# Performance work log

Measured on AMD Instinct MI355X. Metric: run time of the kernel, lower is better.

## Reference

```python
import jax, jax.numpy as jnp
import numpy as np

B, S, HID = 2, 2048, 2048
H, HKV, D = 16, 8, 128
CHUNK = 512
THETA = 1000000.0
NEG = -1e9


def setup_inputs() -> dict:
    key = jax.random.key(0)
    ks = jax.random.split(key, 10)
    hidden_states = jax.random.normal(ks[0], (B, S, HID), dtype=jnp.float32)
    # additive causal mask (0 on/below diagonal, -1e9 above)
    tri = jnp.tril(jnp.ones((S, S), dtype=bool))
    attention_mask = jnp.where(tri, 0.0, NEG).astype(jnp.float32)
    attention_mask = jnp.broadcast_to(attention_mask[None, None], (B, 1, S, S))
    w = 0.02
    Wq = jax.random.normal(ks[1], (HID, H * D), dtype=jnp.float32) * w
    bq = jax.random.normal(ks[2], (H * D,), dtype=jnp.float32) * w
    Wk = jax.random.normal(ks[3], (HID, HKV * D), dtype=jnp.float32) * w
    bk = jax.random.normal(ks[4], (HKV * D,), dtype=jnp.float32) * w
    Wv = jax.random.normal(ks[5], (HID, HKV * D), dtype=jnp.float32) * w
    bv = jax.random.normal(ks[6], (HKV * D,), dtype=jnp.float32) * w
    Wo = jax.random.normal(ks[7], (H * D, HID), dtype=jnp.float32) * w
    bo = jax.random.normal(ks[8], (HID,), dtype=jnp.float32) * w
    return {"hidden_states": hidden_states, "attention_mask": attention_mask,
            "Wq": Wq, "bq": bq, "Wk": Wk, "bk": bk, "Wv": Wv, "bv": bv,
            "Wo": Wo, "bo": bo}


def _rope_tables(seq_len, dim):
    inv_freq = 1.0 / (THETA ** (jnp.arange(0, dim, 2, dtype=jnp.float32) / dim))
    pos = jnp.arange(seq_len, dtype=jnp.float32)
    freqs = pos[:, None] * inv_freq[None, :]          # [S, D/2]
    emb = jnp.concatenate([freqs, freqs], axis=-1)    # [S, D]
    return jnp.cos(emb)[None, None], jnp.sin(emb)[None, None]  # [1,1,S,D]


def _rotate_half(x):
    x1, x2 = jnp.split(x, 2, axis=-1)
    return jnp.concatenate([-x2, x1], axis=-1)


def _attn_forward(hidden_states, attention_mask, Wq, bq, Wk, bk, Wv, bv, Wo, bo):
    bsz, s, _ = hidden_states.shape
    q = (hidden_states @ Wq + bq).reshape(bsz, s, H, D).transpose(0, 2, 1, 3)
    k = (hidden_states @ Wk + bk).reshape(bsz, s, HKV, D).transpose(0, 2, 1, 3)
    v = (hidden_states @ Wv + bv).reshape(bsz, s, HKV, D).transpose(0, 2, 1, 3)
    cos, sin = _rope_tables(s, D)
    q = q * cos + _rotate_half(q) * sin
    k = k * cos + _rotate_half(k) * sin
    n_rep = H // HKV
    k = jnp.repeat(k, n_rep, axis=1)  # repeat_kv
    v = jnp.repeat(v, n_rep, axis=1)
    scale = 1.0 / jnp.sqrt(jnp.float32(D))
    nq, nk = s // CHUNK, s // CHUNK
    Qc = q.reshape(bsz, H, nq, CHUNK, D)
    Kc = jnp.moveaxis(k.reshape(bsz, H, nk, CHUNK, D), 2, 0)   # [nk,B,H,Ck,D]
    Vc = jnp.moveaxis(v.reshape(bsz, H, nk, CHUNK, D), 2, 0)
    Mc = jnp.moveaxis(attention_mask.reshape(bsz, 1, nq, CHUNK, nk, CHUNK), 4, 0)  # [nk,B,1,nq,Cq,Ck]

    def step(carry, xs):
        o, m, d = carry
        k_seg, v_seg, m_seg = xs
        # scores: [B,H,nq,Cq,Ck]
        sc = jnp.einsum('bhqcd,bhkd->bhqck', Qc, k_seg) * scale + m_seg
        new_m = jnp.maximum(m, sc.max(axis=-1, keepdims=True))
        e = jnp.exp(sc - new_m)
        sums = e.sum(axis=-1, keepdims=True)
        prev = jnp.exp(m - new_m)          # NOTE: uses running max, as in source
        d_new = prev + sums
        o = (o * prev + jnp.einsum('bhqck,bhkd->bhqcd', e, v_seg)) / d_new
        return (o, new_m, d_new), None

    o0 = jnp.zeros((bsz, H, nq, CHUNK, D), dtype=jnp.float32)
    m0 = jnp.full((bsz, H, nq, CHUNK, 1), -jnp.inf, dtype=jnp.float32)
    d0 = jnp.ones((bsz, H, nq, CHUNK, 1), dtype=jnp.float32)
    (o, m, d), _ = jax.lax.scan(step, (o0, m0, d0), (Kc, Vc, Mc))
    # final rescale: attn_output * exp(max - logsumexp) == o / d_last (source math)
    o = o / d
    attn = o.reshape(bsz, H, s, D).transpose(0, 2, 1, 3).reshape(bsz, s, H * D)
    return attn @ Wo + bo


def reference(hidden_states, attention_mask, Wq, bq, Wk, bk, Wv, bv, Wo, bo):
    return _attn_forward(hidden_states, attention_mask, Wq, bq, Wk, bk, Wv, bv, Wo, bo)
```

## Files before the change

### kernel.cpp

```cpp
#include <hip/hip_runtime.h>
#include <hip/hip_bf16.h>


typedef __attribute__((ext_vector_type(8))) short s8v;
typedef __attribute__((ext_vector_type(4))) float f4v;
typedef __attribute__((ext_vector_type(4))) unsigned int u32x4;

#define MFMA16(a, b, c) __builtin_amdgcn_mfma_f32_16x16x32_bf16((a), (b), (c), 0, 0, 0)

typedef unsigned short u16;
typedef const __attribute__((address_space(1))) unsigned int* gas_p;
typedef __attribute__((address_space(3))) unsigned int* las_p;

__device__ __forceinline__ void gl_lds16(const void* g, void* l) {
    __builtin_amdgcn_global_load_lds((gas_p)g, (las_p)l, 16, 0, 0);
}

__device__ __forceinline__ u16 f2b(float f) {
    __hip_bfloat16 h = __float2bfloat16(f);
    return *reinterpret_cast<u16*>(&h);
}
__device__ __forceinline__ float b2f(u16 u) {
    __hip_bfloat16 h;
    *reinterpret_cast<u16*>(&h) = u;
    return __bfloat162float(h);
}

__device__ __forceinline__ void qswap(unsigned int& a, unsigned int& b) {
#if __has_builtin(__builtin_amdgcn_permlane32_swap) && __has_builtin(__builtin_amdgcn_permlane16_swap)
    typedef __attribute__((ext_vector_type(2))) unsigned int u32x2;
    u32x2 r1 = __builtin_amdgcn_permlane32_swap(a, b, false, false);
    u32x2 r2 = __builtin_amdgcn_permlane16_swap(r1[0], r1[1], false, false);
    a = r2[0]; b = r2[1];
#else
    asm volatile("v_permlane32_swap_b32 %0, %1\n\t"
                 "s_nop 0\n\t"
                 "v_permlane16_swap_b32 %0, %1\n\t"
                 "s_nop 0"
                 : "+v"(a), "+v"(b));
#endif
}

__device__ const unsigned char qt_tab[40] = {
    4, 5, 6, 7,
    8, 8, 9, 9, 10, 10, 11, 11,
    12, 12, 12, 13, 13, 13, 14, 14, 14, 15, 15, 15,
    3, 7, 11, 15, 2, 6, 10, 14, 1, 5, 9, 13, 0, 4, 8, 12};
__device__ const unsigned char c_tab[40] = {
    0, 0, 0, 0,
    0, 1, 0, 1, 0, 1, 0, 1,
    0, 1, 2, 0, 1, 2, 0, 1, 2, 0, 1, 2,
    0, 1, 2, 3, 0, 1, 2, 3, 0, 1, 2, 3, 0, 1, 2, 3};

__device__ __forceinline__ int uoff40(int qt, int c) {
    int qc = qt >> 2;
    if (c < qc) {
        if (qt < 8) return qt - 4;
        if (qt < 12) return 4 + ((qt - 8) << 1) + c;
        return 12 + (qt - 12) * 3 + c;
    }
    return 24 + ((3 - (qt & 3)) << 2) + qc;
}

__global__ __launch_bounds__(256) void k_cast_hs(const float* __restrict__ src,
                                                 u16* __restrict__ dst) {
    int i = blockIdx.x * 256 + threadIdx.x;
    float4 v = reinterpret_cast<const float4*>(src)[i];
    alignas(8) u16 t[4] = {f2b(v.x), f2b(v.y), f2b(v.z), f2b(v.w)};
    reinterpret_cast<uint2*>(dst)[i] = *reinterpret_cast<uint2*>(t);
}

__global__ __launch_bounds__(256) void k_transpose_w(
    const float* __restrict__ Wq, const float* __restrict__ Wk,
    const float* __restrict__ Wv, const float* __restrict__ Wo,
    u16* __restrict__ wt_all, u16* __restrict__ wo_t) {
    int id = blockIdx.x;
    const float* W; u16* dst; int N, nbase;
    if (id < 4096)      { W = Wq; dst = wt_all; N = 2048; nbase = 0; }
    else if (id < 6144) { W = Wk; dst = wt_all; N = 1024; nbase = 2048; id -= 4096; }
    else if (id < 8192) { W = Wv; dst = wt_all; N = 1024; nbase = 3072; id -= 6144; }
    else                { W = Wo; dst = wo_t;  N = 2048; nbase = 0;    id -= 8192; }
    int tiles_n = N >> 5;
    int k0 = (id / tiles_n) << 5, n0 = (id % tiles_n) << 5;
    __shared__ float t[32][33];
    int tid = threadIdx.x;
    {
        int row = tid >> 3, c4 = (tid & 7) << 2;
        float4 v = *reinterpret_cast<const float4*>(&W[(size_t)(k0 + row) * N + n0 + c4]);
        t[row][c4 + 0] = v.x; t[row][c4 + 1] = v.y;
        t[row][c4 + 2] = v.z; t[row][c4 + 3] = v.w;
    }
    __syncthreads();
    {
        int n = tid >> 3, kq = (tid & 7) << 2;
        alignas(8) u16 p[4];
#pragma unroll
        for (int j = 0; j < 4; j++) p[j] = f2b(t[kq + j][n]);
        *reinterpret_cast<uint2*>(&dst[(size_t)(nbase + n0 + n) * 2048 + k0 + kq]) =
            *reinterpret_cast<uint2*>(p);
    }
}

__global__ __launch_bounds__(256) void k_bias(const float* __restrict__ bq,
                                              const float* __restrict__ bk,
                                              const float* __restrict__ bv,
                                              float* __restrict__ dst) {
    int i = blockIdx.x * 256 + threadIdx.x;
    float v = (i < 2048) ? bq[i] : (i < 3072) ? bk[i - 2048] : bv[i - 3072];
    dst[i] = v;
}

__global__ __launch_bounds__(256) void k_gemm(
    const u16* __restrict__ A, const u16* __restrict__ Bt,
    const float* __restrict__ bias, void* __restrict__ out,
    int M, int N, int K, int out_f32) {
    __shared__ alignas(16) u16 As[128][64];
    __shared__ alignas(16) u16 Bs[128][64];
    int tid = threadIdx.x;
    int wave = tid >> 6, lane = tid & 63, quad = lane >> 4, l16 = lane & 15;
    int m0 = blockIdx.y << 7, n0 = blockIdx.x << 7;
    int wm = (wave >> 1) << 6, wn = (wave & 1) << 6;
    f4v zero = {0.f, 0.f, 0.f, 0.f};
    f4v acc[4][4];
#pragma unroll
    for (int a = 0; a < 4; a++)
#pragma unroll
        for (int b = 0; b < 4; b++) acc[a][b] = zero;
    int r0 = tid >> 3;
    int gsw = (tid & 7) ^ (r0 & 7);
    const u16* gA = A + (size_t)(m0 + r0) * K + (gsw << 3);
    const u16* gB = Bt + (size_t)(n0 + r0) * K + (gsw << 3);
    for (int k0 = 0; k0 < K; k0 += 64) {
        __syncthreads();
#pragma unroll
        for (int i = 0; i < 4; i++) {
            gl_lds16(gA + (size_t)(i << 5) * K + k0, (char*)As + (i << 12) + tid * 16);
            gl_lds16(gB + (size_t)(i << 5) * K + k0, (char*)Bs + (i << 12) + tid * 16);
        }
        __syncthreads();
#pragma unroll
        for (int ks = 0; ks < 2; ks++) {
            int rg = (((ks << 2) | quad) ^ (l16 & 7)) << 3;
            s8v af[4], bf_[4];
#pragma unroll
            for (int mi = 0; mi < 4; mi++)
                af[mi] = *reinterpret_cast<const s8v*>(&As[wm + mi * 16 + l16][rg]);
#pragma unroll
            for (int ni = 0; ni < 4; ni++)
                bf_[ni] = *reinterpret_cast<const s8v*>(&Bs[wn + ni * 16 + l16][rg]);
#pragma unroll
            for (int mi = 0; mi < 4; mi++)
#pragma unroll
                for (int ni = 0; ni < 4; ni++)
                    acc[mi][ni] = MFMA16(af[mi], bf_[ni], acc[mi][ni]);
        }
    }
#pragma unroll
    for (int mi = 0; mi < 4; mi++) {
#pragma unroll
        for (int ni = 0; ni < 4; ni++) {
            int n = n0 + wn + ni * 16 + l16;
            float bsv = bias[n];
#pragma unroll
            for (int r = 0; r < 4; r++) {
                int m = m0 + wm + mi * 16 + (quad << 2) + r;
                float v = acc[mi][ni][r] + bsv;
                if (out_f32)
                    reinterpret_cast<float*>(out)[(size_t)m * N + n] = v;
                else
                    reinterpret_cast<u16*>(out)[(size_t)m * N + n] = f2b(v);
            }
        }
    }
}

__global__ __launch_bounds__(256) void k_rope(const u16* __restrict__ qkv,
                                              u16* __restrict__ qr,
                                              u16* __restrict__ kr) {
    const float qscale = 0.08838834764831845f * 1.44269504088896340f;
    int row = blockIdx.x;
    int b = row >> 11, s = row & 2047;
    const u16* src = qkv + (size_t)row * 4096;
    __shared__ float lcs[64], lsn[64];
    int tid = threadIdx.x;
    if (tid < 64) {
        float fr = (float)s * exp2f((float)tid * -0.31143075889569023f);
        lcs[tid] = cosf(fr);
        lsn[tid] = sinf(fr);
    }
    __syncthreads();
    for (int u = tid; u < 1536; u += 256) {
        int hh, i;
        const u16* sp;
        u16* dp;
        float sc;
        if (u < 1024) {
            hh = u >> 6; i = u & 63;
            sp = src + hh * 128;
            dp = qr + ((size_t)(b * 16 + hh) * 2048 + s) * 128;
            sc = qscale;
        } else {
            int u2 = u - 1024;
            hh = u2 >> 6; i = u2 & 63;
            sp = src + 2048 + hh * 128;
            dp = kr + ((size_t)(b * 8 + hh) * 2048 + s) * 128;
            sc = 1.f;
        }
        float x1 = b2f(sp[i]);
        float x2 = b2f(sp[i + 64]);
        float cs = lcs[i], sn = lsn[i];
        dp[i]      = f2b((x1 * cs - x2 * sn) * sc);
        dp[i + 64] = f2b((x2 * cs + x1 * sn) * sc);
    }
}

__global__ __launch_bounds__(256) void k_vtrans(const u16* __restrict__ qkv,
                                                u16* __restrict__ vt) {
    int bkv = blockIdx.z, b = bkv >> 3, kv = bkv & 7;
    int s0 = blockIdx.x << 6, d0 = blockIdx.y << 5;
    __shared__ alignas(16) u16 t[32][72];
    int tid = threadIdx.x, c = tid & 31, rr = tid >> 5;
#pragma unroll
    for (int i = 0; i < 8; i++) {
        int s = s0 + rr + i * 8;
        t[c][rr + i * 8] = qkv[(size_t)(b * 2048 + s) * 4096 + 3072 + kv * 128 + d0 + c];
    }
    __syncthreads();
    int dd = tid >> 3, sc8 = (tid & 7) << 3;
    *reinterpret_cast<uint4*>(&vt[((size_t)(b * 8 + kv) * 128 + d0 + dd) * 2048 + s0 + sc8]) =
        *reinterpret_cast<const uint4*>(&t[dd][sc8]);
}

__global__ __launch_bounds__(256) void k_attn_part(const u16* __restrict__ qr,
                                                   const u16* __restrict__ kr,
                                                   const u16* __restrict__ vt,
                                                   u16* __restrict__ PVp,
                                                   float* __restrict__ scp) {
    const float NINF = -__builtin_inff();
    __shared__ alignas(16) u16 Ks[2][64 * 128];
    __shared__ alignas(16) u16 Vs[2][128 * 64];

    int tid = threadIdx.x;
    int wv = tid >> 6, lane = tid & 63, quad = lane >> 4, l16 = lane & 15;
    int x = blockIdx.x, h = blockIdx.y, b = blockIdx.z, kvh = h >> 1;
    int qt = qt_tab[x], c = c_tab[x], qc = qt >> 2;
    bool diag = (c == qc);
    int m3 = qt & 3;
    int nt = diag ? ((m3 + 1) << 1) : 8;
    int kbase = c << 9;
    const u16* Qp = qr + ((size_t)(b * 16 + h) * 2048 + qt * 128 + wv * 32) * 128;
    const u16* Kp = kr + ((size_t)(b * 8 + kvh) * 2048) * 128;
    const u16* Vp = vt + ((size_t)(b * 8 + kvh) * 128) * 2048;

    s8v qf0[4], qf1[4];
#pragma unroll
    for (int sl = 0; sl < 4; sl++) {
        qf0[sl] = *reinterpret_cast<const s8v*>(&Qp[l16 * 128 + sl * 32 + (quad << 3)]);
        qf1[sl] = *reinterpret_cast<const s8v*>(&Qp[(16 + l16) * 128 + sl * 32 + (quad << 3)]);
    }
    s8v ones;
#pragma unroll
    for (int i = 0; i < 8; i++) ones[i] = (short)0x3F80;

    int krow = tid >> 4, kg = (tid & 15) ^ krow;
    int vd = tid >> 3, vg = (tid & 7) ^ (vd & 7);
    auto stage = [&](int t) {
        int kbt = kbase + (t << 6);
        const u16* kgp = Kp + (size_t)(kbt + krow) * 128 + (kg << 3);
        const u16* vgp = Vp + (size_t)vd * 2048 + kbt + (vg << 3);
        char* kd = (char*)&Ks[t & 1][0];
        char* vdst = (char*)&Vs[t & 1][0];
#pragma unroll
        for (int i = 0; i < 4; i++) {
            gl_lds16(kgp + (size_t)(i << 4) * 128, kd + (i << 12) + tid * 16);
            gl_lds16(vgp + (size_t)(i << 5) * 2048, vdst + (i << 12) + tid * 16);
        }
    };

    auto pack = [&](const f4v& s, bool tri, bool act, float& tmx,
                    unsigned int& wlo, unsigned int& whi) {
        if (!act) { wlo = 0u; whi = 0u; return; }
        float e[4];
#pragma unroll
        for (int r = 0; r < 4; r++) {
            float v = s[r];
            if (tri && ((quad << 2) + r > l16)) v = NINF;
            tmx = fmaxf(tmx, v);
            e[r] = __builtin_amdgcn_exp2f(v);
        }
        wlo = (unsigned int)f2b(e[0]) | ((unsigned int)f2b(e[1]) << 16);
        whi = (unsigned int)f2b(e[2]) | ((unsigned int)f2b(e[3]) << 16);
    };

    f4v zero = {0.f, 0.f, 0.f, 0.f};
    f4v u0[8], u1[8], sums0 = zero, sums1 = zero;
#pragma unroll
    for (int ni = 0; ni < 8; ni++) { u0[ni] = zero; u1[ni] = zero; }
    float tmx0 = NINF, tmx1 = NINF;
    int qg0 = wv << 1, qg1 = (wv << 1) + 1;

    stage(0);
    for (int t = 0; t < nt; t++) {
        __syncthreads();
        if (t + 1 < nt) stage(t + 1);
        const char* Kbuf = (const char*)&Ks[t & 1][0];
        const char* Vbuf = (const char*)&Vs[t & 1][0];
        int kgb = diag ? ((t << 2) - (m3 << 3)) : -1000;

#pragma unroll
        for (int s2 = 0; s2 < 2; s2++) {
            int kgA = kgb + (s2 << 1);
            if (kgA > qg1) continue;
            int kgB = kgA + 1;
            bool a0 = (kgA <= qg0), b0 = (kgB <= qg0), b1 = (kgB <= qg1);
            f4v sA0 = zero, sA1 = zero, sB0 = zero, sB1 = zero;
#pragma unroll
            for (int sl = 0; sl < 4; sl++) {
                s8v kf = *reinterpret_cast<const s8v*>(
                    Kbuf + (((s2 << 1) << 4) + l16) * 256 +
                    ((((sl << 2) + quad) ^ l16) << 4));
                if (a0) sA0 = MFMA16(kf, qf0[sl], sA0);
                sA1 = MFMA16(kf, qf1[sl], sA1);
            }
            if (b1) {
#pragma unroll
                for (int sl = 0; sl < 4; sl++) {
                    s8v kf = *reinterpret_cast<const s8v*>(
                        Kbuf + ((((s2 << 1) | 1) << 4) + l16) * 256 +
                        ((((sl << 2) + quad) ^ l16) << 4));
                    if (b0) sB0 = MFMA16(kf, qf0[sl], sB0);
                    sB1 = MFMA16(kf, qf1[sl], sB1);
                }
            }
            unsigned int A0w, A1w, B0w, B1w;
            pack(sA1, kgA == qg1, true, tmx1, A0w, A1w);
            pack(sB1, kgB == qg1, b1, tmx1, B0w, B1w);
            qswap(A0w, B0w); qswap(A1w, B1w);
            u32x4 pw1 = {A0w, A1w, B0w, B1w};
            s8v pa1 = __builtin_bit_cast(s8v, pw1);
            sums1 = MFMA16(pa1, ones, sums1);
            s8v pa0 = pa1;
            if (a0) {
                unsigned int C0w, C1w, D0w, D1w;
                pack(sA0, kgA == qg0, true, tmx0, C0w, C1w);
                pack(sB0, kgB == qg0, b0, tmx0, D0w, D1w);
                qswap(C0w, D0w); qswap(C1w, D1w);
                u32x4 pw0 = {C0w, C1w, D0w, D1w};
                pa0 = __builtin_bit_cast(s8v, pw0);
                sums0 = MFMA16(pa0, ones, sums0);
            }
#pragma unroll
            for (int ni = 0; ni < 8; ni++) {
                s8v vf = *reinterpret_cast<const s8v*>(
                    Vbuf + ((ni << 4) + l16) * 128 +
                    ((((s2 << 2) + quad) ^ (l16 & 7)) << 4));
                if (a0) u0[ni] = MFMA16(pa0, vf, u0[ni]);
                u1[ni] = MFMA16(pa1, vf, u1[ni]);
            }
        }
    }
    tmx0 = fmaxf(tmx0, __shfl_xor(tmx0, 16));
    tmx0 = fmaxf(tmx0, __shfl_xor(tmx0, 32));
    tmx1 = fmaxf(tmx1, __shfl_xor(tmx1, 16));
    tmx1 = fmaxf(tmx1, __shfl_xor(tmx1, 32));
    float m0[4], m1[4], resc0[4], resc1[4];
#pragma unroll
    for (int r = 0; r < 4; r++) {
        m0[r] = __shfl(tmx0, (quad << 2) + r);
        m1[r] = __shfl(tmx1, (quad << 2) + r);
        resc0[r] = __builtin_amdgcn_exp2f(-m0[r]);
        resc1[r] = __builtin_amdgcn_exp2f(-m1[r]);
    }
    int slot = (b * 16 + h) * 40 + x;
    u16* pvdst = PVp + (size_t)slot * 16384;
    int row0 = wv * 32 + (quad << 2);
#pragma unroll
    for (int ni = 0; ni < 8; ni++)
#pragma unroll
        for (int r = 0; r < 4; r++) {
            pvdst[(row0 + r) * 128 + ni * 16 + l16] = f2b(u0[ni][r] * resc0[r]);
            pvdst[(row0 + 16 + r) * 128 + ni * 16 + l16] = f2b(u1[ni][r] * resc1[r]);
        }
    if (l16 == 0) {
        float* scd = scp + (size_t)slot * 256 + row0;
#pragma unroll
        for (int r = 0; r < 4; r++) {
            scd[r] = m0[r] * 0.6931471805599453f;
            scd[16 + r] = m1[r] * 0.6931471805599453f;
            scd[128 + r] = sums0[r] * resc0[r];
            scd[144 + r] = sums1[r] * resc1[r];
        }
    }
}

__global__ __launch_bounds__(256) void k_attn_comb(const u16* __restrict__ PVp,
                                                   const float* __restrict__ scp,
                                                   u16* __restrict__ attnb) {
    int qt64 = blockIdx.x, h = blockIdx.y, b = blockIdx.z;
    int qt = qt64 >> 1, qc = qt >> 2;
    int tid = threadIdx.x;
    int row = ((qt64 & 1) << 6) + (tid >> 2), d0 = (tid & 3) << 5;
    int bh = b * 16 + h;
    float o[32];
#pragma unroll
    for (int i = 0; i < 32; i++) o[i] = 0.f;
    float mprev = -__builtin_inff(), dlast = 1.f;
    for (int cc = 0; cc <= qc; cc++) {
        int slot = bh * 40 + uoff40(qt, cc);
        float ch = scp[(size_t)slot * 256 + row];
        float sh = scp[(size_t)slot * 256 + 128 + row];
        float mnew = fmaxf(mprev, ch);
        float p = __expf(mprev - mnew);
        float lam = __expf(ch - mnew);
        float dd = p + lam * sh;
        float inv = 1.f / dd;
        const u16* pv = PVp + (size_t)slot * 16384 + row * 128 + d0;
#pragma unroll
        for (int k = 0; k < 4; k++) {
            s8v v8 = *reinterpret_cast<const s8v*>(pv + (k << 3));
#pragma unroll
            for (int j = 0; j < 8; j++) {
                int i = (k << 3) + j;
                o[i] = (o[i] * p + lam * b2f((u16)v8[j])) * inv;
            }
        }
        mprev = mnew;
        dlast = dd;
    }
    if (qc == 3) {
        float inv = 1.f / dlast;
#pragma unroll
        for (int i = 0; i < 32; i++) o[i] *= inv;
    }
    alignas(16) u16 ob[32];
#pragma unroll
    for (int i = 0; i < 32; i++) ob[i] = f2b(o[i]);
    u16* dst = attnb + (size_t)(b * 2048 + qt * 128 + row) * 2048 + h * 128 + d0;
#pragma unroll
    for (int k = 0; k < 4; k++)
        reinterpret_cast<uint4*>(dst)[k] = reinterpret_cast<const uint4*>(ob)[k];
}

extern "C" void kernel_launch(void* const* d_in, const int* in_sizes, int n_in,
                              void* d_out, int out_size, void* d_ws, size_t ws_size,
                              hipStream_t stream) {
    (void)in_sizes; (void)n_in; (void)out_size; (void)ws_size;
    const float* hs = (const float*)d_in[0];
    const float* Wq = (const float*)d_in[2];
    const float* bq = (const float*)d_in[3];
    const float* Wk = (const float*)d_in[4];
    const float* bk = (const float*)d_in[5];
    const float* Wv = (const float*)d_in[6];
    const float* bv = (const float*)d_in[7];
    const float* Wo = (const float*)d_in[8];
    const float* bo = (const float*)d_in[9];

    char* ws = (char*)d_ws;
    u16* hsb      = (u16*)(ws);
    u16* qr       = hsb;
    u16* attnb    = hsb;
    u16* wt_all   = (u16*)(ws + (16u << 20));
    u16* kr       = wt_all;
    u16* vt       = (u16*)(ws + (24u << 20));
    u16* wo_t     = (u16*)(ws + (32u << 20));
    float* bias_c = (float*)(ws + (40u << 20));
    u16* qkv      = (u16*)(ws + (40u << 20) + 65536);
    u16* PVp      = qkv;
    float* scp    = (float*)(ws + (40u << 20) + 65536 + 41943040u);

    k_cast_hs<<<8192, 256, 0, stream>>>(hs, hsb);
    k_transpose_w<<<12288, 256, 0, stream>>>(Wq, Wk, Wv, Wo, wt_all, wo_t);
    k_bias<<<16, 256, 0, stream>>>(bq, bk, bv, bias_c);
    k_gemm<<<dim3(32, 32), 256, 0, stream>>>(hsb, wt_all, bias_c, qkv,
                                             4096, 4096, 2048, 0);
    k_rope<<<4096, 256, 0, stream>>>(qkv, qr, kr);
    k_vtrans<<<dim3(32, 4, 16), 256, 0, stream>>>(qkv, vt);
    k_attn_part<<<dim3(40, 16, 2), 256, 0, stream>>>(qr, kr, vt, PVp, scp);
    k_attn_comb<<<dim3(32, 16, 2), 256, 0, stream>>>(PVp, scp, attnb);
    k_gemm<<<dim3(16, 32), 256, 0, stream>>>(attnb, wo_t, bo, d_out,
                                             4096, 2048, 2048, 1);
}
```

Baseline: 417.4 us.

## Single-buffer V in LDS, split QK and PV phases, template diag path

The attention-partial kernel now keeps only one V tile in LDS instead of two, which cuts its shared-memory footprint, and requests three blocks per CU through launch_bounds. Each iteration first computes QK scores and packs P for both sub-steps while V loads in flight, then synchronises and runs the PV and row-sum MFMAs. The diagonal and off-diagonal tiles are compiled as separate template instantiations so the masking branches fold away on full tiles. The trade-off is an extra barrier per iteration, V loads that are no longer prefetched a tile ahead, and more live registers holding the packed P fragments under a tighter register budget.

```diff
diff --git a/kernel.cpp b/kernel.cpp
--- a/kernel.cpp
+++ b/kernel.cpp
@@ -11,6 +11,8 @@
 typedef unsigned short u16;
 typedef const __attribute__((address_space(1))) unsigned int* gas_p;
 typedef __attribute__((address_space(3))) unsigned int* las_p;
+
+template <bool B> struct BoolC { static constexpr bool value = B; };
 
 __device__ __forceinline__ void gl_lds16(const void* g, void* l) {
     __builtin_amdgcn_global_load_lds((gas_p)g, (las_p)l, 16, 0, 0);
@@ -231,14 +233,14 @@
         *reinterpret_cast<const uint4*>(&t[dd][sc8]);
 }
 
-__global__ __launch_bounds__(256) void k_attn_part(const u16* __restrict__ qr,
-                                                   const u16* __restrict__ kr,
-                                                   const u16* __restrict__ vt,
-                                                   u16* __restrict__ PVp,
-                                                   float* __restrict__ scp) {
+__global__ __launch_bounds__(256, 3) void k_attn_part(const u16* __restrict__ qr,
+                                                      const u16* __restrict__ kr,
+                                                      const u16* __restrict__ vt,
+                                                      u16* __restrict__ PVp,
+                                                      float* __restrict__ scp) {
     const float NINF = -__builtin_inff();
     __shared__ alignas(16) u16 Ks[2][64 * 128];
-    __shared__ alignas(16) u16 Vs[2][128 * 64];
+    __shared__ alignas(16) u16 Vs[128 * 64];
 
     int tid = threadIdx.x;
     int wv = tid >> 6, lane = tid & 63, quad = lane >> 4, l16 = lane & 15;
@@ -261,20 +263,27 @@
     s8v ones;
 #pragma unroll
     for (int i = 0; i < 8; i++) ones[i] = (short)0x3F80;
+    s8v pzero;
+#pragma unroll
+    for (int i = 0; i < 8; i++) pzero[i] = (short)0;
 
     int krow = tid >> 4, kg = (tid & 15) ^ krow;
     int vd = tid >> 3, vg = (tid & 7) ^ (vd & 7);
-    auto stage = [&](int t) {
+    auto stageK = [&](int t) {
         int kbt = kbase + (t << 6);
         const u16* kgp = Kp + (size_t)(kbt + krow) * 128 + (kg << 3);
+        char* kd = (char*)&Ks[t & 1][0];
+#pragma unroll
+        for (int i = 0; i < 4; i++)
+            gl_lds16(kgp + (size_t)(i << 4) * 128, kd + (i << 12) + tid * 16);
+    };
+    auto stageV = [&](int t) {
+        int kbt = kbase + (t << 6);
         const u16* vgp = Vp + (size_t)vd * 2048 + kbt + (vg << 3);
-        char* kd = (char*)&Ks[t & 1][0];
-        char* vdst = (char*)&Vs[t & 1][0];
-#pragma unroll
-        for (int i = 0; i < 4; i++) {
-            gl_lds16(kgp + (size_t)(i << 4) * 128, kd + (i << 12) + tid * 16);
+        char* vdst = (char*)&Vs[0];
+#pragma unroll
+        for (int i = 0; i < 4; i++)
             gl_lds16(vgp + (size_t)(i << 5) * 2048, vdst + (i << 12) + tid * 16);
-        }
     };
 
     auto pack = [&](const f4v& s, bool tri, bool act, float& tmx,
@@ -299,66 +308,83 @@
     float tmx0 = NINF, tmx1 = NINF;
     int qg0 = wv << 1, qg1 = (wv << 1) + 1;
 
-    stage(0);
-    for (int t = 0; t < nt; t++) {
-        __syncthreads();
-        if (t + 1 < nt) stage(t + 1);
-        const char* Kbuf = (const char*)&Ks[t & 1][0];
-        const char* Vbuf = (const char*)&Vs[t & 1][0];
-        int kgb = diag ? ((t << 2) - (m3 << 3)) : -1000;
-
-#pragma unroll
-        for (int s2 = 0; s2 < 2; s2++) {
-            int kgA = kgb + (s2 << 1);
-            if (kgA > qg1) continue;
-            int kgB = kgA + 1;
-            bool a0 = (kgA <= qg0), b0 = (kgB <= qg0), b1 = (kgB <= qg1);
-            f4v sA0 = zero, sA1 = zero, sB0 = zero, sB1 = zero;
-#pragma unroll
-            for (int sl = 0; sl < 4; sl++) {
-                s8v kf = *reinterpret_cast<const s8v*>(
-                    Kbuf + (((s2 << 1) << 4) + l16) * 256 +
-                    ((((sl << 2) + quad) ^ l16) << 4));
-                if (a0) sA0 = MFMA16(kf, qf0[sl], sA0);
-                sA1 = MFMA16(kf, qf1[sl], sA1);
-            }
-            if (b1) {
+    auto run = [&](auto diagc) {
+        constexpr bool DIAG = decltype(diagc)::value;
+        stageK(0);
+        for (int t = 0; t < nt; t++) {
+            __syncthreads();
+            stageV(t);
+            if (t + 1 < nt) stageK(t + 1);
+            const char* Kbuf = (const char*)&Ks[t & 1][0];
+            int kgb = DIAG ? ((t << 2) - (m3 << 3)) : 0;
+            s8v pa0s[2], pa1s[2];
+            bool act0[2], act1[2];
+#pragma unroll
+            for (int s2 = 0; s2 < 2; s2++) {
+                int kgA = kgb + (s2 << 1), kgB = kgA + 1;
+                bool skip = DIAG && (kgA > qg1);
+                bool a0 = !DIAG || (kgA <= qg0);
+                bool b0 = !DIAG || (kgB <= qg0);
+                bool b1 = !DIAG || (kgB <= qg1);
+                act1[s2] = !skip;
+                act0[s2] = !skip && a0;
+                if (skip) { pa0s[s2] = pzero; pa1s[s2] = pzero; continue; }
+                f4v sA0 = zero, sA1 = zero, sB0 = zero, sB1 = zero;
 #pragma unroll
                 for (int sl = 0; sl < 4; sl++) {
                     s8v kf = *reinterpret_cast<const s8v*>(
-                        Kbuf + ((((s2 << 1) | 1) << 4) + l16) * 256 +
+                        Kbuf + (((s2 << 1) << 4) + l16) * 256 +
                         ((((sl << 2) + quad) ^ l16) << 4));
-                    if (b0) sB0 = MFMA16(kf, qf0[sl], sB0);
-                    sB1 = MFMA16(kf, qf1[sl], sB1);
+                    if (a0) sA0 = MFMA16(kf, qf0[sl], sA0);
+                    sA1 = MFMA16(kf, qf1[sl], sA1);
+                }
+                if (b1) {
+#pragma unroll
+                    for (int sl = 0; sl < 4; sl++) {
+                        s8v kf = *reinterpret_cast<const s8v*>(
+                            Kbuf + ((((s2 << 1) | 1) << 4) + l16) * 256 +
+                            ((((sl << 2) + quad) ^ l16) << 4));
+                        if (b0) sB0 = MFMA16(kf, qf0[sl], sB0);
+                        sB1 = MFMA16(kf, qf1[sl], sB1);
+                    }
+                }
+                unsigned int A0w, A1w, B0w, B1w;
+                pack(sA1, DIAG && (kgA == qg1), true, tmx1, A0w, A1w);
+                pack(sB1, DIAG && (kgB == qg1), b1, tmx1, B0w, B1w);
+                qswap(A0w, B0w); qswap(A1w, B1w);
+                u32x4 pw1 = {A0w, A1w, B0w, B1w};
+                pa1s[s2] = __builtin_bit_cast(s8v, pw1);
+                if (a0) {
+                    unsigned int C0w, C1w, D0w, D1w;
+                    pack(sA0, DIAG && (kgA == qg0), true, tmx0, C0w, C1w);
+                    pack(sB0, DIAG && (kgB == qg0), b0, tmx0, D0w, D1w);
+                    qswap(C0w, D0w); qswap(C1w, D1w);
+                    u32x4 pw0 = {C0w, C1w, D0w, D1w};
+                    pa0s[s2] = __builtin_bit_cast(s8v, pw0);
+                } else {
+                    pa0s[s2] = pa1s[s2];
                 }
             }
-            unsigned int A0w, A1w, B0w, B1w;
-            pack(sA1, kgA == qg1, true, tmx1, A0w, A1w);
-            pack(sB1, kgB == qg1, b1, tmx1, B0w, B1w);
-            qswap(A0w, B0w); qswap(A1w, B1w);
-            u32x4 pw1 = {A0w, A1w, B0w, B1w};
-            s8v pa1 = __builtin_bit_cast(s8v, pw1);
-            sums1 = MFMA16(pa1, ones, sums1);
-            s8v pa0 = pa1;
-            if (a0) {
-                unsigned int C0w, C1w, D0w, D1w;
-                pack(sA0, kgA == qg0, true, tmx0, C0w, C1w);
-                pack(sB0, kgB == qg0, b0, tmx0, D0w, D1w);
-                qswap(C0w, D0w); qswap(C1w, D1w);
-                u32x4 pw0 = {C0w, C1w, D0w, D1w};
-                pa0 = __builtin_bit_cast(s8v, pw0);
-                sums0 = MFMA16(pa0, ones, sums0);
+            __syncthreads();
+#pragma unroll
+            for (int s2 = 0; s2 < 2; s2++) {
+                if (DIAG && !act1[s2]) continue;
+                bool a0 = !DIAG || act0[s2];
+                if (a0) sums0 = MFMA16(pa0s[s2], ones, sums0);
+                sums1 = MFMA16(pa1s[s2], ones, sums1);
+#pragma unroll
+                for (int ni = 0; ni < 8; ni++) {
+                    s8v vf = *reinterpret_cast<const s8v*>(
+                        (const char*)&Vs[0] + ((ni << 4) + l16) * 128 +
+                        ((((s2 << 2) + quad) ^ (l16 & 7)) << 4));
+                    if (a0) u0[ni] = MFMA16(pa0s[s2], vf, u0[ni]);
+                    u1[ni] = MFMA16(pa1s[s2], vf, u1[ni]);
+                }
             }
-#pragma unroll
-            for (int ni = 0; ni < 8; ni++) {
-                s8v vf = *reinterpret_cast<const s8v*>(
-                    Vbuf + ((ni << 4) + l16) * 128 +
-                    ((((s2 << 2) + quad) ^ (l16 & 7)) << 4));
-                if (a0) u0[ni] = MFMA16(pa0, vf, u0[ni]);
-                u1[ni] = MFMA16(pa1, vf, u1[ni]);
-            }
-        }
-    }
+        }
+    };
+    if (diag) run(BoolC<true>{}); else run(BoolC<false>{});
+
     tmx0 = fmaxf(tmx0, __shfl_xor(tmx0, 16));
     tmx0 = fmaxf(tmx0, __shfl_xor(tmx0, 32));
     tmx1 = fmaxf(tmx1, __shfl_xor(tmx1, 16));
```

New measurement: 378.1 us. 9.4% less time.
